# Kernel tuning notes

Measured on AMD Instinct MI355X. Metric: run time of the kernel, lower is better.

The kernel has to match this reference:

```python
import jax, jax.numpy as jnp
import numpy as np

EPS = 1e-12  # tf/keras l2_normalize epsilon


def _hadamard(n):
    # Sylvester construction; n must be a power of 2
    H = np.array([[1.0]], dtype=np.float32)
    while H.shape[0] < n:
        H = np.block([[H, H], [H, -H]])
    return H


def setup_inputs() -> dict:
    key = jax.random.key(0)
    k1, k2 = jax.random.split(key)
    in_dim, out_dim, batch = 2048, 16384, 1024
    hadamard_size = 16384  # next pow2 of max(in_dim, out_dim)
    H = _hadamard(hadamard_size)[:in_dim, :out_dim]  # [2048, 16384]
    init_scale = 1.0 / np.sqrt(out_dim)
    x = jax.random.normal(k1, (batch, in_dim), dtype=jnp.float32)
    scale = jnp.full((1,), init_scale, dtype=jnp.float32)
    bias = jax.random.uniform(k2, (out_dim,), minval=-init_scale, maxval=init_scale, dtype=jnp.float32)
    return {"x": x, "scale": scale, "bias": bias, "hadamard": jnp.asarray(H)}


def reference(x, scale, bias, hadamard):
    # L2-normalize along features (keras: x / sqrt(max(sum(x^2), eps)))
    sq = jnp.sum(x * x, axis=-1, keepdims=True)
    xn = x * jax.lax.rsqrt(jnp.maximum(sq, EPS))
    # structured Hadamard matmul (expressed as dense GEMM, as in the original)
    out = -scale * jnp.matmul(xn, hadamard)  # [B, out_dim]
    out = out + bias
    return out
```

## Files before the change

### kernel.cpp

```cpp
#include <hip/hip_runtime.h>

#define IN_DIM   2048
#define OUT_DIM  16384
#define NTHREADS 256
#define EPS      1e-12f

__global__ __launch_bounds__(NTHREADS) void had_fwht_kernel(
    const float* __restrict__ x,
    const float* __restrict__ scale,
    const float* __restrict__ bias,
    float* __restrict__ out)
{
    __shared__ float s[IN_DIM];
    __shared__ float red[NTHREADS / 64];

    const int b   = blockIdx.x;
    const int tid = threadIdx.x;

    const float4* xr4 = (const float4*)(x + (size_t)b * IN_DIM);
    float local = 0.f;
#pragma unroll
    for (int i = 0; i < IN_DIM / 4 / NTHREADS; ++i) {
        const int idx = tid + i * NTHREADS;
        float4 v = xr4[idx];
        ((float4*)s)[idx] = v;
        local = fmaf(v.x, v.x, local);
        local = fmaf(v.y, v.y, local);
        local = fmaf(v.z, v.z, local);
        local = fmaf(v.w, v.w, local);
    }

#pragma unroll
    for (int off = 32; off > 0; off >>= 1)
        local += __shfl_down(local, off, 64);
    if ((tid & 63) == 0) red[tid >> 6] = local;
    __syncthreads();
    const float sumsq = red[0] + red[1] + red[2] + red[3];
    const float c = -scale[0] * rsqrtf(fmaxf(sumsq, EPS));

#pragma unroll
    for (int d = 1; d < IN_DIM; d <<= 1) {
#pragma unroll
        for (int t = tid; t < IN_DIM / 2; t += NTHREADS) {
            const int i = ((t & ~(d - 1)) << 1) | (t & (d - 1));
            const float a  = s[i];
            const float bb = s[i + d];
            s[i]     = a + bb;
            s[i + d] = a - bb;
        }
        __syncthreads();
    }

    const float4* bias4 = (const float4*)bias;
    const float4* s4    = (const float4*)s;
    float4* out4        = (float4*)(out + (size_t)b * OUT_DIM);
#pragma unroll
    for (int i = 0; i < OUT_DIM / 4 / NTHREADS; ++i) {
        const int idx = tid + i * NTHREADS;
        const float4 bv = bias4[idx];
        const float4 sv = s4[idx & (IN_DIM / 4 - 1)];
        float4 o;
        o.x = fmaf(c, sv.x, bv.x);
        o.y = fmaf(c, sv.y, bv.y);
        o.z = fmaf(c, sv.z, bv.z);
        o.w = fmaf(c, sv.w, bv.w);
        out4[idx] = o;
    }
}

extern "C" void kernel_launch(void* const* d_in, const int* in_sizes, int n_in,
                              void* d_out, int out_size, void* d_ws, size_t ws_size,
                              hipStream_t stream) {
    const float* x     = (const float*)d_in[0];
    const float* scale = (const float*)d_in[1];
    const float* bias  = (const float*)d_in[2];
    float* out = (float*)d_out;

    const int batch = in_sizes[0] / IN_DIM;
    had_fwht_kernel<<<batch, NTHREADS, 0, stream>>>(x, scale, bias, out);
}
```

Before: 21.22 us.

## Register-blocked radix-8 FWHT with swizzled shared memory to cut barrier count

Replaces the 11-stage shared-memory butterfly loop with a register-blocked radix-8 FWHT where each thread holds 8 values and performs three butterfly levels per pass, so only four shared-memory exchanges and barriers are needed. An XOR swizzle on shared-memory indices is meant to avoid bank conflicts in the strided passes, and the final result goes to a second buffer. This reduces synchronization and LDS traffic per row at the cost of an extra 8 KB of shared memory and more intricate indexing.

After: 18.61 us. -12.3%, faster.

```diff
diff --git a/kernel.cpp b/kernel.cpp
--- a/kernel.cpp
+++ b/kernel.cpp
@@ -2,61 +2,90 @@
 
 #define IN_DIM   2048
 #define OUT_DIM  16384
-#define NTHREADS 256
+#define NT       256
 #define EPS      1e-12f
 
-__global__ __launch_bounds__(NTHREADS) void had_fwht_kernel(
+
+__device__ __forceinline__ int swz(int e) { return e ^ (((e >> 6) & 7) << 3); }
+
+#define BFLY(m)                                                   \
+    _Pragma("unroll")                                             \
+    for (int k = 0; k < 8; ++k)                                   \
+        if (!(k & (m))) {                                         \
+            const float a_ = v[k], b_ = v[k | (m)];               \
+            v[k]       = a_ + b_;                                 \
+            v[k | (m)] = a_ - b_;                                 \
+        }
+
+__global__ __launch_bounds__(NT) void had_fwht_kernel(
     const float* __restrict__ x,
     const float* __restrict__ scale,
     const float* __restrict__ bias,
     float* __restrict__ out)
 {
-    __shared__ float s[IN_DIM];
-    __shared__ float red[NTHREADS / 64];
+    __shared__ float sA[IN_DIM];
+    __shared__ float sB[IN_DIM];
+    __shared__ float red[NT / 64];
 
-    const int b   = blockIdx.x;
-    const int tid = threadIdx.x;
+    const int b = blockIdx.x;
+    const int t = threadIdx.x;
+    float v[8];
 
     const float4* xr4 = (const float4*)(x + (size_t)b * IN_DIM);
+    const float4 a0 = xr4[2 * t];
+    const float4 a1 = xr4[2 * t + 1];
+    v[0] = a0.x; v[1] = a0.y; v[2] = a0.z; v[3] = a0.w;
+    v[4] = a1.x; v[5] = a1.y; v[6] = a1.z; v[7] = a1.w;
+
     float local = 0.f;
 #pragma unroll
-    for (int i = 0; i < IN_DIM / 4 / NTHREADS; ++i) {
-        const int idx = tid + i * NTHREADS;
-        float4 v = xr4[idx];
-        ((float4*)s)[idx] = v;
-        local = fmaf(v.x, v.x, local);
-        local = fmaf(v.y, v.y, local);
-        local = fmaf(v.z, v.z, local);
-        local = fmaf(v.w, v.w, local);
-    }
-
+    for (int k = 0; k < 8; ++k) local = fmaf(v[k], v[k], local);
 #pragma unroll
     for (int off = 32; off > 0; off >>= 1)
         local += __shfl_down(local, off, 64);
-    if ((tid & 63) == 0) red[tid >> 6] = local;
+    if ((t & 63) == 0) red[t >> 6] = local;
+
+    BFLY(1) BFLY(2) BFLY(4)
+    ((float4*)sA)[swz(8 * t)     >> 2] = make_float4(v[0], v[1], v[2], v[3]);
+    ((float4*)sA)[swz(8 * t + 4) >> 2] = make_float4(v[4], v[5], v[6], v[7]);
     __syncthreads();
+
     const float sumsq = red[0] + red[1] + red[2] + red[3];
     const float c = -scale[0] * rsqrtf(fmaxf(sumsq, EPS));
 
+    {
+        const int base = (t & 7) | ((t >> 3) << 6);
 #pragma unroll
-    for (int d = 1; d < IN_DIM; d <<= 1) {
+        for (int k = 0; k < 8; ++k) v[k] = sA[swz(base | (k << 3))];
+        BFLY(1) BFLY(2) BFLY(4)
 #pragma unroll
-        for (int t = tid; t < IN_DIM / 2; t += NTHREADS) {
-            const int i = ((t & ~(d - 1)) << 1) | (t & (d - 1));
-            const float a  = s[i];
-            const float bb = s[i + d];
-            s[i]     = a + bb;
-            s[i + d] = a - bb;
-        }
-        __syncthreads();
+        for (int k = 0; k < 8; ++k) sA[swz(base | (k << 3))] = v[k];
     }
+    __syncthreads();
+
+    {
+        const int base = (t & 63) | ((t >> 6) << 9);
+#pragma unroll
+        for (int k = 0; k < 8; ++k) v[k] = sA[swz(base | (k << 6))];
+        BFLY(1) BFLY(2)
+#pragma unroll
+        for (int k = 0; k < 8; ++k) sA[swz(base | (k << 6))] = v[k];
+    }
+    __syncthreads();
+
+#pragma unroll
+    for (int k = 0; k < 8; ++k) v[k] = sA[swz(t | (k << 8))];
+    BFLY(1) BFLY(2) BFLY(4)
+#pragma unroll
+    for (int k = 0; k < 8; ++k) sB[t | (k << 8)] = v[k];
+    __syncthreads();
 
     const float4* bias4 = (const float4*)bias;
-    const float4* s4    = (const float4*)s;
+    const float4* s4    = (const float4*)sB;
     float4* out4        = (float4*)(out + (size_t)b * OUT_DIM);
 #pragma unroll
-    for (int i = 0; i < OUT_DIM / 4 / NTHREADS; ++i) {
-        const int idx = tid + i * NTHREADS;
+    for (int i = 0; i < OUT_DIM / 4 / NT; ++i) {
+        const int idx = t + i * NT;
         const float4 bv = bias4[idx];
         const float4 sv = s4[idx & (IN_DIM / 4 - 1)];
         float4 o;
@@ -77,5 +106,5 @@
     float* out = (float*)d_out;
 
     const int batch = in_sizes[0] / IN_DIM;
-    had_fwht_kernel<<<batch, NTHREADS, 0, stream>>>(x, scale, bias, out);
+    had_fwht_kernel<<<batch, NT, 0, stream>>>(x, scale, bias, out);
 }
```

## Compute per-row Walsh-Hadamard transform in registers with one wavefront per row

Applied to the files above, without the earlier changes.

Replaces the 256-thread shared-memory FWHT with a single 64-lane wavefront per batch row. Each lane keeps 32 elements in registers. The butterflies run over register indices in-thread and over lane bits via xor shuffles. This removes the LDS traffic and the eleven block barriers of the transform stage, and the sum-of-squares reduction becomes a pure shuffle reduction. In exchange each CU gets fewer threads for the store-heavy output phase, which may limit how well memory latency is hidden while writing the large output.

Result: no change. 21.17 us (-0.2%).

```diff
diff --git a/kernel.cpp b/kernel.cpp
--- a/kernel.cpp
+++ b/kernel.cpp
@@ -2,69 +2,75 @@
 
 #define IN_DIM   2048
 #define OUT_DIM  16384
-#define NTHREADS 256
 #define EPS      1e-12f
 
-__global__ __launch_bounds__(NTHREADS) void had_fwht_kernel(
+
+__global__ __launch_bounds__(64) void had_wave_kernel(
     const float* __restrict__ x,
     const float* __restrict__ scale,
     const float* __restrict__ bias,
     float* __restrict__ out)
 {
-    __shared__ float s[IN_DIM];
-    __shared__ float red[NTHREADS / 64];
+    const int row = blockIdx.x;
+    const int l   = threadIdx.x;
 
-    const int b   = blockIdx.x;
-    const int tid = threadIdx.x;
+    const float4* xr4 = (const float4*)(x + (size_t)row * IN_DIM);
+    float v[32];
+#pragma unroll
+    for (int k4 = 0; k4 < 8; ++k4) {
+        const float4 L = xr4[(k4 << 6) | l];
+        v[k4 * 4 + 0] = L.x;
+        v[k4 * 4 + 1] = L.y;
+        v[k4 * 4 + 2] = L.z;
+        v[k4 * 4 + 3] = L.w;
+    }
 
-    const float4* xr4 = (const float4*)(x + (size_t)b * IN_DIM);
     float local = 0.f;
 #pragma unroll
-    for (int i = 0; i < IN_DIM / 4 / NTHREADS; ++i) {
-        const int idx = tid + i * NTHREADS;
-        float4 v = xr4[idx];
-        ((float4*)s)[idx] = v;
-        local = fmaf(v.x, v.x, local);
-        local = fmaf(v.y, v.y, local);
-        local = fmaf(v.z, v.z, local);
-        local = fmaf(v.w, v.w, local);
+    for (int r = 0; r < 32; ++r) local = fmaf(v[r], v[r], local);
+#pragma unroll
+    for (int m = 1; m < 64; m <<= 1)
+        local += __shfl_xor(local, m, 64);
+    const float c = -scale[0] * rsqrtf(fmaxf(local, EPS));
+
+#pragma unroll
+    for (int m = 1; m < 32; m <<= 1) {
+#pragma unroll
+        for (int r = 0; r < 32; ++r)
+            if (!(r & m)) {
+                const float a_ = v[r], b_ = v[r | m];
+                v[r]     = a_ + b_;
+                v[r | m] = a_ - b_;
+            }
     }
 
 #pragma unroll
-    for (int off = 32; off > 0; off >>= 1)
-        local += __shfl_down(local, off, 64);
-    if ((tid & 63) == 0) red[tid >> 6] = local;
-    __syncthreads();
-    const float sumsq = red[0] + red[1] + red[2] + red[3];
-    const float c = -scale[0] * rsqrtf(fmaxf(sumsq, EPS));
+    for (int m = 1; m < 64; m <<= 1) {
+#pragma unroll
+        for (int r = 0; r < 32; ++r) {
+            const float o = __shfl_xor(v[r], m, 64);
+            v[r] = (l & m) ? (o - v[r]) : (v[r] + o);
+        }
+    }
 
 #pragma unroll
-    for (int d = 1; d < IN_DIM; d <<= 1) {
-#pragma unroll
-        for (int t = tid; t < IN_DIM / 2; t += NTHREADS) {
-            const int i = ((t & ~(d - 1)) << 1) | (t & (d - 1));
-            const float a  = s[i];
-            const float bb = s[i + d];
-            s[i]     = a + bb;
-            s[i + d] = a - bb;
-        }
-        __syncthreads();
-    }
+    for (int r = 0; r < 32; ++r) v[r] *= c;
 
     const float4* bias4 = (const float4*)bias;
-    const float4* s4    = (const float4*)s;
-    float4* out4        = (float4*)(out + (size_t)b * OUT_DIM);
+    float4* out4        = (float4*)(out + (size_t)row * OUT_DIM);
 #pragma unroll
-    for (int i = 0; i < OUT_DIM / 4 / NTHREADS; ++i) {
-        const int idx = tid + i * NTHREADS;
-        const float4 bv = bias4[idx];
-        const float4 sv = s4[idx & (IN_DIM / 4 - 1)];
-        float4 o;
-        o.x = fmaf(c, sv.x, bv.x);
-        o.y = fmaf(c, sv.y, bv.y);
-        o.z = fmaf(c, sv.z, bv.z);
-        o.w = fmaf(c, sv.w, bv.w);
-        out4[idx] = o;
+    for (int cpy = 0; cpy < 8; ++cpy) {
+#pragma unroll
+        for (int k4 = 0; k4 < 8; ++k4) {
+            const int idx = cpy * 512 + (k4 << 6) + l;
+            const float4 bv = bias4[idx & 4095];
+            float4 o;
+            o.x = v[k4 * 4 + 0] + bv.x;
+            o.y = v[k4 * 4 + 1] + bv.y;
+            o.z = v[k4 * 4 + 2] + bv.z;
+            o.w = v[k4 * 4 + 3] + bv.w;
+            out4[idx] = o;
+        }
     }
 }
 
@@ -77,5 +83,5 @@
     float* out = (float*)d_out;
 
     const int batch = in_sizes[0] / IN_DIM;
-    had_fwht_kernel<<<batch, NTHREADS, 0, stream>>>(x, scale, bias, out);
+    had_wave_kernel<<<batch, 64, 0, stream>>>(x, scale, bias, out);
 }
```
